# Kernel tuning notes

Measured on AMD Instinct MI355X. Metric: run time of the kernel, lower is better.

Reference implementation:

```python
import jax, jax.numpy as jnp
import numpy as np

B, S, HID = 4, 1024, 1024
H, HK, D = 16, 8, 64
EPS = 1e-6
THETA = 10000.0
ROPE_SCALE = 1.0


def _rms_norm(x, gamma=None):
    # RMSNorm over head_dim; Gemma-style (1+gamma) scale, v_norm has no scale.
    v = x * jax.lax.rsqrt(jnp.mean(x * x, axis=-1, keepdims=True) + EPS)
    return v if gamma is None else v * (1.0 + gamma)


def _rope_1d(x, pos, theta, scale):
    # x: [B,S,h,d], pos: [B,S] -> rotate-half RoPE along d
    d = x.shape[-1]
    inv_freq = 1.0 / (theta ** (jnp.arange(0, d, 2, dtype=jnp.float32) / d))  # [d/2]
    ang = (pos.astype(jnp.float32) / scale)[..., None] * inv_freq             # [B,S,d/2]
    cos = jnp.cos(ang)[:, :, None, :]
    sin = jnp.sin(ang)[:, :, None, :]
    x1, x2 = x[..., : d // 2], x[..., d // 2 :]
    return jnp.concatenate([x1 * cos - x2 * sin, x2 * cos + x1 * sin], axis=-1)


def _multidim_rope(x, positions_xy, theta, scale):
    # split head_dim in half: first half rotated by x-position, second by y-position
    d = x.shape[-1]
    xh, yh = x[..., : d // 2], x[..., d // 2 :]
    return jnp.concatenate(
        [_rope_1d(xh, positions_xy[..., 0], theta, scale),
         _rope_1d(yh, positions_xy[..., 1], theta, scale)], axis=-1)


def setup_inputs() -> dict:
    key = jax.random.key(0)
    ks = jax.random.split(key, 8)
    std = 0.02
    return {
        "hidden_states": jax.random.normal(ks[0], (B, S, HID), jnp.float32),
        "Wq": jax.random.normal(ks[1], (HID, H * D), jnp.float32) * std,
        "Wk": jax.random.normal(ks[2], (HID, HK * D), jnp.float32) * std,
        "Wv": jax.random.normal(ks[3], (HID, HK * D), jnp.float32) * std,
        "Wo": jax.random.normal(ks[4], (H * D, HID), jnp.float32) * std,
        "q_gamma": jax.random.normal(ks[5], (D,), jnp.float32) * 0.02,
        "k_gamma": jax.random.normal(ks[6], (D,), jnp.float32) * 0.02,
        "positions_xy": jax.random.randint(ks[7], (B, S, 2), 0, 32, dtype=jnp.int32),
        "attention_mask": jnp.ones((B, S, S), dtype=bool),
    }


def reference(hidden_states, Wq, Wk, Wv, Wo, q_gamma, k_gamma, positions_xy, attention_mask):
    b, s, _ = hidden_states.shape
    q = (hidden_states @ Wq).reshape(b, s, H, D)
    k = (hidden_states @ Wk).reshape(b, s, HK, D)
    v = (hidden_states @ Wv).reshape(b, s, HK, D)
    q = _rms_norm(q, q_gamma)
    k = _rms_norm(k, k_gamma)
    v = _rms_norm(v)  # no scale
    q = _multidim_rope(q, positions_xy, THETA, ROPE_SCALE).transpose(0, 2, 1, 3)  # [B,H,S,D]
    k = _multidim_rope(k, positions_xy, THETA, ROPE_SCALE).transpose(0, 2, 1, 3)  # [B,HK,S,D]
    v = v.transpose(0, 2, 1, 3)                                                   # [B,HK,S,D]
    groups = H // HK
    k = jnp.repeat(k, groups, axis=1)  # GQA expand -> [B,H,S,D]
    v = jnp.repeat(v, groups, axis=1)
    # scale=1.0 per the original SDPA call (no 1/sqrt(d))
    logits = jnp.einsum("bhqd,bhkd->bhqk", q, k)
    neg = jnp.asarray(jnp.finfo(logits.dtype).min, logits.dtype)
    logits = jnp.where(attention_mask[:, None, :, :], logits, neg)
    probs = jax.nn.softmax(logits.astype(jnp.float32), axis=-1).astype(q.dtype)
    out = jnp.einsum("bhqk,bhkd->bhqd", probs, v)
    out = out.transpose(0, 2, 1, 3).reshape(b, s, H * D)
    return out @ Wo
```

## Files before the change

kernel.cpp:

```cpp
#include <hip/hip_runtime.h>
#include <hip/hip_bf16.h>
#include <stdint.h>

typedef __attribute__((ext_vector_type(8))) short short8;
typedef __attribute__((ext_vector_type(4))) float f32x4;
typedef __attribute__((ext_vector_type(16))) float f32x16;

#define MFMA16(a, b, c) __builtin_amdgcn_mfma_f32_16x16x32_bf16(a, b, c, 0, 0, 0)
#define MFMA32(a, b, c) __builtin_amdgcn_mfma_f32_32x32x16_bf16(a, b, c, 0, 0, 0)

__device__ __forceinline__ unsigned short f2bf_u(float f) {
  union { float f; uint32_t u; } x; x.f = f;
  uint32_t r = (x.u + 0x7fffu + ((x.u >> 16) & 1u)) >> 16;
  return (unsigned short)r;
}
__device__ __forceinline__ short f2bf(float f) { return (short)f2bf_u(f); }

__device__ __forceinline__ uint32_t pack_bf2(float lo, float hi) {
  __hip_bfloat162 h = __float22bfloat162_rn(make_float2(lo, hi));
  union { __hip_bfloat162 h; uint32_t u; } c; c.h = h;
  return c.u;
}

__device__ __forceinline__ void gload_lds16(const void* g, void* lds) {
  __builtin_amdgcn_global_load_lds(
      (const __attribute__((address_space(1))) uint32_t*)(uintptr_t)g,
      (__attribute__((address_space(3))) uint32_t*)(uintptr_t)lds,
      16, 0, 0);
}

__global__ __launch_bounds__(256) void convert_bf16_kernel(
    const float* __restrict__ in, short* __restrict__ out, int n4) {
  int i = blockIdx.x * 256 + threadIdx.x;
  if (i >= n4) return;
  float4 v = reinterpret_cast<const float4*>(in)[i];
  short4 o;
  o.x = f2bf(v.x); o.y = f2bf(v.y); o.z = f2bf(v.z); o.w = f2bf(v.w);
  reinterpret_cast<short4*>(out)[i] = o;
}

__global__ __launch_bounds__(256) void transpose_all_kernel(
    const float* __restrict__ Wq, const float* __restrict__ Wk,
    const float* __restrict__ Wv, const float* __restrict__ Wo,
    short* __restrict__ WTQKV, short* __restrict__ WOT) {
  __shared__ float tile[32][33];
  int yb = blockIdx.y;
  const float* src; short* dst; int N; int yy;
  if (yb < 32)      { src = Wq; dst = WTQKV;                       N = 1024; yy = yb; }
  else if (yb < 48) { src = Wk; dst = WTQKV + (size_t)1024 * 1024; N = 512;  yy = yb - 32; }
  else if (yb < 64) { src = Wv; dst = WTQKV + (size_t)1536 * 1024; N = 512;  yy = yb - 48; }
  else              { src = Wo; dst = WOT;                         N = 1024; yy = yb - 64; }
  int k0 = blockIdx.x * 32, n0 = yy * 32;
  int tx = threadIdx.x, ty = threadIdx.y;
#pragma unroll
  for (int i = 0; i < 4; ++i)
    tile[ty + 8 * i][tx] = src[(size_t)(k0 + ty + 8 * i) * N + n0 + tx];
  __syncthreads();
#pragma unroll
  for (int i = 0; i < 4; ++i)
    dst[(size_t)(n0 + ty + 8 * i) * 1024 + k0 + tx] = f2bf(tile[tx][ty + 8 * i]);
}

__global__ __launch_bounds__(256) void gemm_qkv_fused(
    const short* __restrict__ A, const short* __restrict__ BT,
    const float* __restrict__ qg, const float* __restrict__ kg,
    const int* __restrict__ pos,
    short* __restrict__ Qp, short* __restrict__ Kp, short* __restrict__ Vt) {
  const int K = 1024;
  __shared__ short As[2 * 128 * 32];
  __shared__ short Bs[2 * 128 * 32];
  int wg = blockIdx.x + gridDim.x * blockIdx.y;
  int lid = (wg & 7) * 64 + (wg >> 3);
  int m0 = (lid & 31) * 128, n0 = (lid >> 5) * 128;
  int t = threadIdx.x;
  int w = t >> 6, lane = t & 63;
  int wr = w >> 1, wc = w & 1;
  int lr = lane & 15, lg = lane >> 4;

  f32x4 acc[4][4] = {};

  for (int k0 = 0; k0 < K; k0 += 64) {
    __syncthreads();
#pragma unroll
    for (int i = 0; i < 4; ++i) {
      int q = t + 256 * i;
      int kk = q >> 9, row = (q >> 2) & 127, c = q & 3;
      gload_lds16(A + (size_t)(m0 + row) * K + k0 + kk * 32 + c * 8, &As[q * 8]);
      gload_lds16(BT + (size_t)(n0 + row) * K + k0 + kk * 32 + c * 8, &Bs[q * 8]);
    }
    __syncthreads();
#pragma unroll
    for (int kk = 0; kk < 2; ++kk) {
      short8 af[4], bf[4];
#pragma unroll
      for (int mi = 0; mi < 4; ++mi)
        af[mi] = *(const short8*)&As[kk * 4096 + (wr * 64 + mi * 16 + lr) * 32 + lg * 8];
#pragma unroll
      for (int ni = 0; ni < 4; ++ni)
        bf[ni] = *(const short8*)&Bs[kk * 4096 + (wc * 64 + ni * 16 + lr) * 32 + lg * 8];
      __builtin_amdgcn_s_setprio(1);
#pragma unroll
      for (int mi = 0; mi < 4; ++mi)
#pragma unroll
        for (int ni = 0; ni < 4; ++ni)
          acc[mi][ni] = MFMA16(af[mi], bf[ni], acc[mi][ni]);
      __builtin_amdgcn_s_setprio(0);
    }
  }

  int g = (n0 >> 6) + wc;
  int row0 = m0 + wr * 64;
  const int2* posv = (const int2*)pos;

  if (g < 24) {
    const float* gsrc = (g < 16) ? qg : kg;
    short* dst = (g < 16) ? Qp : Kp;
    int nh = (g < 16) ? 16 : 8;
    int h = (g < 16) ? g : g - 16;
    float gscale = (g < 16) ? 1.4426950408889634f : 1.0f;
    float gam[4];
#pragma unroll
    for (int ni = 0; ni < 4; ++ni) gam[ni] = (1.0f + gsrc[ni * 16 + lr]) * gscale;
    float invf = exp2f((float)lr * -0.8304820237218405f);
#pragma unroll
    for (int mi = 0; mi < 4; ++mi) {
      f32x4 ss = acc[mi][0] * acc[mi][0];
#pragma unroll
      for (int ni = 1; ni < 4; ++ni) ss += acc[mi][ni] * acc[mi][ni];
#pragma unroll
      for (int m2 = 1; m2 < 16; m2 <<= 1)
#pragma unroll
        for (int r = 0; r < 4; ++r) ss[r] += __shfl_xor(ss[r], m2);
#pragma unroll
      for (int r = 0; r < 4; ++r) {
        int row = row0 + mi * 16 + lg * 4 + r;
        float inv = rsqrtf(ss[r] * 0.015625f + 1e-6f);
        float v0 = acc[mi][0][r] * inv * gam[0];
        float v1 = acc[mi][1][r] * inv * gam[1];
        float v2 = acc[mi][2][r] * inv * gam[2];
        float v3 = acc[mi][3][r] * inv * gam[3];
        int2 pp = posv[row];
        float sx, cx, sy, cy;
        __sincosf((float)pp.x * invf, &sx, &cx);
        __sincosf((float)pp.y * invf, &sy, &cy);
        float o0 = v0 * cx - v1 * sx, o1 = v1 * cx + v0 * sx;
        float o2 = v2 * cy - v3 * sy, o3 = v3 * cy + v2 * sy;
        int s = row & 1023, bb = row >> 10;
        short* base = dst + ((size_t)((bb * nh + h) * 1024 + s)) * 64;
        base[lr]      = f2bf(o0);
        base[lr + 16] = f2bf(o1);
        base[lr + 32] = f2bf(o2);
        base[lr + 48] = f2bf(o3);
      }
    }
  } else {
    int hk = g - 24;
#pragma unroll
    for (int mi = 0; mi < 4; ++mi) {
      f32x4 ss = acc[mi][0] * acc[mi][0];
#pragma unroll
      for (int ni = 1; ni < 4; ++ni) ss += acc[mi][ni] * acc[mi][ni];
#pragma unroll
      for (int m2 = 1; m2 < 16; m2 <<= 1)
#pragma unroll
        for (int r = 0; r < 4; ++r) ss[r] += __shfl_xor(ss[r], m2);
      f32x4 inv;
#pragma unroll
      for (int r = 0; r < 4; ++r) inv[r] = rsqrtf(ss[r] * 0.015625f + 1e-6f);
      int row = row0 + mi * 16 + lg * 4;
      int s0 = row & 1023, bb = row >> 10;
      int kv = s0 & 63, c = kv >> 3, hb = (kv >> 2) & 1;
      int sp = (s0 & ~63) | (((c & 6) | hb) << 3) | ((c & 1) << 2);
#pragma unroll
      for (int ni = 0; ni < 4; ++ni) {
        short4 sv;
        sv.x = f2bf(acc[mi][ni][0] * inv[0]);
        sv.y = f2bf(acc[mi][ni][1] * inv[1]);
        sv.z = f2bf(acc[mi][ni][2] * inv[2]);
        sv.w = f2bf(acc[mi][ni][3] * inv[3]);
        int d = ni * 16 + lr;
        *(short4*)&Vt[((size_t)((bb * 8 + hk) * 64 + d)) * 1024 + sp] = sv;
      }
    }
  }
}

__global__ __launch_bounds__(256) void gemm_bf16_bn64(
    const short* __restrict__ A, const short* __restrict__ BT,
    float* __restrict__ C, int M, int N, int K) {
  __shared__ short As[2 * 128 * 32];
  __shared__ short Bs[2 * 64 * 32];
  int wg = blockIdx.x + gridDim.x * blockIdx.y;
  int lid = (wg & 7) * 64 + (wg >> 3);
  int m0 = (lid & 31) * 128, n0 = (lid >> 5) * 64;
  int t = threadIdx.x;
  int w = t >> 6, lane = t & 63;
  int lr = lane & 15, lg = lane >> 4;

  f32x4 acc[2][4] = {};

  for (int k0 = 0; k0 < K; k0 += 64) {
    __syncthreads();
#pragma unroll
    for (int i = 0; i < 4; ++i) {
      int q = t + 256 * i;
      int kk = q >> 9, row = (q >> 2) & 127, c = q & 3;
      gload_lds16(A + (size_t)(m0 + row) * K + k0 + kk * 32 + c * 8, &As[q * 8]);
    }
#pragma unroll
    for (int i = 0; i < 2; ++i) {
      int q = t + 256 * i;
      int kk = q >> 8, row = (q >> 2) & 63, c = q & 3;
      gload_lds16(BT + (size_t)(n0 + row) * K + k0 + kk * 32 + c * 8, &Bs[q * 8]);
    }
    __syncthreads();
#pragma unroll
    for (int kk = 0; kk < 2; ++kk) {
      short8 af[2], bf[4];
#pragma unroll
      for (int mi = 0; mi < 2; ++mi)
        af[mi] = *(const short8*)&As[kk * 4096 + (w * 32 + mi * 16 + lr) * 32 + lg * 8];
#pragma unroll
      for (int ni = 0; ni < 4; ++ni)
        bf[ni] = *(const short8*)&Bs[kk * 2048 + (ni * 16 + lr) * 32 + lg * 8];
      __builtin_amdgcn_s_setprio(1);
#pragma unroll
      for (int mi = 0; mi < 2; ++mi)
#pragma unroll
        for (int ni = 0; ni < 4; ++ni)
          acc[mi][ni] = MFMA16(af[mi], bf[ni], acc[mi][ni]);
      __builtin_amdgcn_s_setprio(0);
    }
  }
#pragma unroll
  for (int mi = 0; mi < 2; ++mi)
#pragma unroll
    for (int ni = 0; ni < 4; ++ni) {
      int row = m0 + w * 32 + mi * 16 + lg * 4;
      int col = n0 + ni * 16 + lr;
#pragma unroll
      for (int r = 0; r < 4; ++r)
        C[(size_t)(row + r) * N + col] = acc[mi][ni][r];
    }
}

__global__ __launch_bounds__(256, 2) void attn_kernel(
    const short* __restrict__ Qp, const short* __restrict__ Kp,
    const short* __restrict__ Vt, short* __restrict__ attn) {
  __shared__ char smem[65536];
  __shared__ float lsl[2][32][2];
  int wg = blockIdx.x;
  int xcd = wg & 7, slot = wg >> 3;
  int group = xcd * 8 + (slot >> 4);
  int qblk = slot & 15;
  int b = group >> 4, h = group & 15;
  int hk = h >> 1;
  int t = threadIdx.x;
  int w = t >> 6, lane = t & 63;
  int qw = w >> 1, kw = w & 1;
  int l31 = lane & 31, hh = lane >> 5;
  int xr = l31 & 7;
  int q0 = qblk * 64 + qw * 32;

  const short* Qb = Qp + ((size_t)(b * 16 + h) * 1024) * 64;
  const short* Kb = Kp + ((size_t)(b * 8 + hk) * 1024) * 64;
  const short* Vb = Vt + ((size_t)(b * 8 + hk) * 64) * 1024;

  short8 qf[4];
#pragma unroll
  for (int dk = 0; dk < 4; ++dk)
    qf[dk] = *(const short8*)&Qb[(q0 + l31) * 64 + dk * 16 + hh * 8];

  f32x16 acc[2] = {};
  f32x4 lsumv = {};

  auto KsB = [&](int buf) { return (short*)(smem + (size_t)(kw * 2 + buf) * 8192); };
  auto VsB = [&](int buf) { return (short*)(smem + 32768 + (size_t)(kw * 2 + buf) * 8192); };

  auto STAGE = [&](int buf, int kt) {
    int kv0 = kw * 512 + kt * 64;
    short* ksb = KsB(buf);
    short* vsb = VsB(buf);
#pragma unroll
    for (int i = 0; i < 4; ++i) {
      int c = i * 128 + qw * 64 + lane;
      int kv = c >> 3, cd = c & 7, cs = cd ^ (kv & 7);
      gload_lds16(Kb + (size_t)(kv0 + kv) * 64 + cs * 8, &ksb[c * 8]);
    }
#pragma unroll
    for (int i = 0; i < 4; ++i) {
      int c = i * 128 + qw * 64 + lane;
      int d = c >> 3, bi = c & 7, bs = bi ^ (d & 7);
      gload_lds16(Vb + (size_t)d * 1024 + kv0 + bs * 8, &vsb[c * 8]);
    }
  };

  auto COMPUTE = [&](int buf) {
    const short* ksb = KsB(buf);
    const short* vsb = VsB(buf);
#pragma unroll
    for (int kvb2 = 0; kvb2 < 2; ++kvb2) {
      short8 kf[4];
#pragma unroll
      for (int dk = 0; dk < 4; ++dk)
        kf[dk] = *(const short8*)&ksb[(kvb2 * 32 + l31) * 64 + ((dk * 2 + hh) ^ xr) * 8];
      f32x16 sv = {};
      __builtin_amdgcn_s_setprio(1);
#pragma unroll
      for (int dk = 0; dk < 4; ++dk) sv = MFMA32(kf[dk], qf[dk], sv);
      __builtin_amdgcn_s_setprio(0);
      short8 vf[4];
#pragma unroll
      for (int kvc = 0; kvc < 2; ++kvc)
#pragma unroll
        for (int db2 = 0; db2 < 2; ++db2)
          vf[kvc * 2 + db2] = *(const short8*)
              &vsb[(db2 * 32 + l31) * 64 + (((kvb2 * 4 + kvc * 2 + hh) ^ xr)) * 8];
      float p[16];
#pragma unroll
      for (int r = 0; r < 16; ++r) p[r] = exp2f(sv[r]);
#pragma unroll
      for (int r = 0; r < 16; r += 4) {
        lsumv[0] += p[r]; lsumv[1] += p[r + 1];
        lsumv[2] += p[r + 2]; lsumv[3] += p[r + 3];
      }
      uint32_t pk8[8];
#pragma unroll
      for (int j = 0; j < 8; ++j) pk8[j] = pack_bf2(p[2 * j], p[2 * j + 1]);
#pragma unroll
      for (int kvc = 0; kvc < 2; ++kvc) {
        union { uint32_t u[4]; short8 s; } pb;
#pragma unroll
        for (int j = 0; j < 4; ++j) pb.u[j] = pk8[kvc * 4 + j];
        __builtin_amdgcn_s_setprio(1);
#pragma unroll
        for (int db2 = 0; db2 < 2; ++db2)
          acc[db2] = MFMA32(vf[kvc * 2 + db2], pb.s, acc[db2]);
        __builtin_amdgcn_s_setprio(0);
      }
    }
  };

  STAGE(0, 0);
  int cur = 0;
  for (int kt = 0; kt < 7; ++kt) {
    STAGE(cur ^ 1, kt + 1);
    asm volatile("s_waitcnt vmcnt(8)" ::: "memory");
    __builtin_amdgcn_s_barrier();
    __builtin_amdgcn_sched_barrier(0);
    COMPUTE(cur);
    __builtin_amdgcn_sched_barrier(0);
    __builtin_amdgcn_s_barrier();
    cur ^= 1;
  }
  asm volatile("s_waitcnt vmcnt(0)" ::: "memory");
  __builtin_amdgcn_s_barrier();
  COMPUTE(cur);

  float lsum = (lsumv[0] + lsumv[1]) + (lsumv[2] + lsumv[3]);
  __syncthreads();
  float* accl = (float*)smem;
  float* ab = accl + (((qw * 32 + l31) * 2 + hh) * 36);
  if (kw == 1) {
#pragma unroll
    for (int db2 = 0; db2 < 2; ++db2)
#pragma unroll
      for (int j4 = 0; j4 < 4; ++j4) {
        f32x4 sv4;
        sv4[0] = acc[db2][j4 * 4];
        sv4[1] = acc[db2][j4 * 4 + 1];
        sv4[2] = acc[db2][j4 * 4 + 2];
        sv4[3] = acc[db2][j4 * 4 + 3];
        *(f32x4*)&ab[db2 * 16 + j4 * 4] = sv4;
      }
    lsl[qw][l31][hh] = lsum;
  }
  __syncthreads();
  if (kw == 0) {
#pragma unroll
    for (int db2 = 0; db2 < 2; ++db2)
#pragma unroll
      for (int j4 = 0; j4 < 4; ++j4) {
        f32x4 o = *(const f32x4*)&ab[db2 * 16 + j4 * 4];
        acc[db2][j4 * 4]     += o[0];
        acc[db2][j4 * 4 + 1] += o[1];
        acc[db2][j4 * 4 + 2] += o[2];
        acc[db2][j4 * 4 + 3] += o[3];
      }
    lsum += lsl[qw][l31][hh];
    lsum += __shfl_xor(lsum, 32);
    float inv = 1.0f / lsum;
    short* orow = attn + ((size_t)(b * 1024 + q0 + l31)) * 1024 + h * 64;
#pragma unroll
    for (int db2 = 0; db2 < 2; ++db2)
#pragma unroll
      for (int g2 = 0; g2 < 4; ++g2) {
        int d0 = db2 * 32 + g2 * 8 + 4 * hh;
        uint32_t w0 = pack_bf2(acc[db2][g2 * 4 + 0] * inv, acc[db2][g2 * 4 + 1] * inv);
        uint32_t w1 = pack_bf2(acc[db2][g2 * 4 + 2] * inv, acc[db2][g2 * 4 + 3] * inv);
        *(uint2*)&orow[d0] = make_uint2(w0, w1);
      }
  }
}

extern "C" void kernel_launch(void* const* d_in, const int* in_sizes, int n_in,
                              void* d_out, int out_size, void* d_ws, size_t ws_size,
                              hipStream_t stream) {
  const float* X  = (const float*)d_in[0];
  const float* Wq = (const float*)d_in[1];
  const float* Wk = (const float*)d_in[2];
  const float* Wv = (const float*)d_in[3];
  const float* Wo = (const float*)d_in[4];
  const float* qg = (const float*)d_in[5];
  const float* kg = (const float*)d_in[6];
  const int* pos  = (const int*)d_in[7];
  float* out = (float*)d_out;

  char* ws = (char*)d_ws;
  short* XB    = (short*)(ws);
  short* WTQKV = (short*)(ws + ((size_t)8 << 20));
  short* WOT   = (short*)(ws + ((size_t)12 << 20));
  short* QP    = (short*)(ws + ((size_t)14 << 20));
  short* KP    = (short*)(ws + ((size_t)22 << 20));
  short* VT    = (short*)(ws + ((size_t)26 << 20));
  short* ATT   = (short*)(ws + ((size_t)30 << 20));

  convert_bf16_kernel<<<4096, 256, 0, stream>>>(X, XB, 1048576);
  transpose_all_kernel<<<dim3(32, 96), dim3(32, 8), 0, stream>>>(Wq, Wk, Wv, Wo, WTQKV, WOT);

  gemm_qkv_fused<<<dim3(32, 16), 256, 0, stream>>>(XB, WTQKV, qg, kg, pos, QP, KP, VT);
  attn_kernel<<<1024, 256, 0, stream>>>(QP, KP, VT, ATT);
  gemm_bf16_bn64<<<dim3(32, 16), 256, 0, stream>>>(ATT, WOT, out, 4096, 1024, 1024);
}
```

Baseline: 99.24 us.

## Load V fragments directly from global memory and use hardware exp2

Stops staging V tiles through LDS with async global-to-LDS copies; each wave now reads its V fragments straight from global memory inside the compute loop. LDS shrinks to the K double buffers only, and the wait count drops to match the smaller number of in-flight loads. exp2f is also swapped for the raw hardware exp2 builtin. The aim is to cut LDS footprint and staging traffic, but it puts global-load latency directly in the MFMA path and duplicates V reads across the query waves.

Result: slower. 109.4 us (+10.3%).

```diff
diff --git a/kernel.cpp b/kernel.cpp
--- a/kernel.cpp
+++ b/kernel.cpp
@@ -20,6 +20,10 @@
   __hip_bfloat162 h = __float22bfloat162_rn(make_float2(lo, hi));
   union { __hip_bfloat162 h; uint32_t u; } c; c.h = h;
   return c.u;
+}
+
+__device__ __forceinline__ float fexp2(float x) {
+  return __builtin_amdgcn_exp2f(x);
 }
 
 __device__ __forceinline__ void gload_lds16(const void* g, void* lds) {
@@ -247,7 +251,7 @@
 __global__ __launch_bounds__(256, 2) void attn_kernel(
     const short* __restrict__ Qp, const short* __restrict__ Kp,
     const short* __restrict__ Vt, short* __restrict__ attn) {
-  __shared__ char smem[65536];
+  __shared__ short Ks[4][4096];
   __shared__ float lsl[2][32][2];
   int wg = blockIdx.x;
   int xcd = wg & 7, slot = wg >> 3;
@@ -274,30 +278,20 @@
   f32x16 acc[2] = {};
   f32x4 lsumv = {};
 
-  auto KsB = [&](int buf) { return (short*)(smem + (size_t)(kw * 2 + buf) * 8192); };
-  auto VsB = [&](int buf) { return (short*)(smem + 32768 + (size_t)(kw * 2 + buf) * 8192); };
-
   auto STAGE = [&](int buf, int kt) {
     int kv0 = kw * 512 + kt * 64;
-    short* ksb = KsB(buf);
-    short* vsb = VsB(buf);
+    short* ksb = &Ks[kw * 2 + buf][0];
 #pragma unroll
     for (int i = 0; i < 4; ++i) {
       int c = i * 128 + qw * 64 + lane;
       int kv = c >> 3, cd = c & 7, cs = cd ^ (kv & 7);
       gload_lds16(Kb + (size_t)(kv0 + kv) * 64 + cs * 8, &ksb[c * 8]);
     }
-#pragma unroll
-    for (int i = 0; i < 4; ++i) {
-      int c = i * 128 + qw * 64 + lane;
-      int d = c >> 3, bi = c & 7, bs = bi ^ (d & 7);
-      gload_lds16(Vb + (size_t)d * 1024 + kv0 + bs * 8, &vsb[c * 8]);
-    }
   };
 
-  auto COMPUTE = [&](int buf) {
-    const short* ksb = KsB(buf);
-    const short* vsb = VsB(buf);
+  auto COMPUTE = [&](int buf, int kt) {
+    const short* ksb = &Ks[kw * 2 + buf][0];
+    int kv0 = kw * 512 + kt * 64;
 #pragma unroll
     for (int kvb2 = 0; kvb2 < 2; ++kvb2) {
       short8 kf[4];
@@ -315,10 +309,10 @@
 #pragma unroll
         for (int db2 = 0; db2 < 2; ++db2)
           vf[kvc * 2 + db2] = *(const short8*)
-              &vsb[(db2 * 32 + l31) * 64 + (((kvb2 * 4 + kvc * 2 + hh) ^ xr)) * 8];
+              &Vb[(size_t)(db2 * 32 + l31) * 1024 + kv0 + (kvb2 * 4 + kvc * 2 + hh) * 8];
       float p[16];
 #pragma unroll
-      for (int r = 0; r < 16; ++r) p[r] = exp2f(sv[r]);
+      for (int r = 0; r < 16; ++r) p[r] = fexp2(sv[r]);
 #pragma unroll
       for (int r = 0; r < 16; r += 4) {
         lsumv[0] += p[r]; lsumv[1] += p[r + 1];
@@ -345,21 +339,21 @@
   int cur = 0;
   for (int kt = 0; kt < 7; ++kt) {
     STAGE(cur ^ 1, kt + 1);
-    asm volatile("s_waitcnt vmcnt(8)" ::: "memory");
+    asm volatile("s_waitcnt vmcnt(4)" ::: "memory");
     __builtin_amdgcn_s_barrier();
     __builtin_amdgcn_sched_barrier(0);
-    COMPUTE(cur);
+    COMPUTE(cur, kt);
     __builtin_amdgcn_sched_barrier(0);
     __builtin_amdgcn_s_barrier();
     cur ^= 1;
   }
   asm volatile("s_waitcnt vmcnt(0)" ::: "memory");
   __builtin_amdgcn_s_barrier();
-  COMPUTE(cur);
+  COMPUTE(cur, 7);
 
   float lsum = (lsumv[0] + lsumv[1]) + (lsumv[2] + lsumv[3]);
   __syncthreads();
-  float* accl = (float*)smem;
+  float* accl = (float*)&Ks[0][0];
   float* ab = accl + (((qw * 32 + l31) * 2 + hh) * 36);
   if (kw == 1) {
 #pragma unroll
```
